# Performance work log

Measured on AMD Instinct MI355X. Metric: run time of the kernel, lower is better.

Reference implementation:

```python
import jax, jax.numpy as jnp
import numpy as np

B, S_IN, S_OUT, D_IN, D_OUT = 8, 1024, 1024, 256, 256
LN_EPS = 1e-5
TWO_PI = 2.0 * np.pi


def setup_inputs() -> dict:
    key = jax.random.key(0)
    ks = jax.random.split(key, 6)
    x = jax.random.normal(ks[0], (B, S_IN, D_IN), dtype=jnp.float32)
    M = jax.random.uniform(ks[1], (D_OUT, D_IN), minval=-0.5, maxval=0.5, dtype=jnp.float32)
    P = jax.random.uniform(ks[2], (D_OUT, D_OUT), minval=-0.1, maxval=0.1, dtype=jnp.float32)
    Linker = jax.random.uniform(ks[3], (S_IN, S_OUT), minval=-0.1, maxval=0.1, dtype=jnp.float32)
    ln_gamma = 1.0 + 0.1 * jax.random.normal(ks[4], (D_OUT,), dtype=jnp.float32)
    ln_beta = 0.1 * jax.random.normal(ks[5], (D_OUT,), dtype=jnp.float32)
    # periods[i, j] = i * out_dim + j + 2  (fixed buffer, non-trainable)
    i = jnp.arange(D_OUT, dtype=jnp.float32)[:, None]
    j = jnp.arange(D_OUT, dtype=jnp.float32)[None, :]
    periods = i * D_OUT + j + 2.0
    return {"x": x, "M": M, "P": P, "Linker": Linker,
            "ln_gamma": ln_gamma, "ln_beta": ln_beta, "periods": periods}


def _layer_norm(z, gamma, beta):
    mu = jnp.mean(z, axis=-1, keepdims=True)
    var = jnp.mean(jnp.square(z - mu), axis=-1, keepdims=True)
    return (z - mu) * jax.lax.rsqrt(var + LN_EPS) * gamma + beta


def reference(x, M, P, Linker, ln_gamma, ln_beta, periods):
    # Projection + LayerNorm: Z [B, S, D]
    Zl = jnp.matmul(x, M.T)
    Z = _layer_norm(Zl, ln_gamma, ln_beta)

    # Position-dependent cos-phase gated reduction:
    # T[b,k,i] = sum_j Z[b,k,j] * P[i,j] * cos(2*pi*k / periods[i,j])
    k = jnp.arange(Z.shape[1], dtype=jnp.float32)  # [S]
    phi = jnp.cos(TWO_PI * k[:, None, None] / periods[None, :, :])  # [S, D, D]
    T = jnp.einsum('bkj,ij,kij->bki', Z, P, phi)

    # Sequence transform via Linker: U[b,s,d] = sum_k T[b,k,d] * Linker[k,s]
    U = jnp.einsum('bkd,ks->bsd', T, Linker)

    # Shared residual: (x @ M^T) through the same Linker
    residual = jnp.einsum('bkd,ks->bsd', Zl, Linker)
    return U + residual
```

## Files before the change

### kernel.cpp

```cpp
#include <hip/hip_runtime.h>
#include <math.h>

#define NB   8
#define SEQ  1024
#define DIM  256

static constexpr float LN_EPS_C = 1e-5f;

typedef __bf16 bfx8 __attribute__((ext_vector_type(8)));
typedef __bf16 bfx4 __attribute__((ext_vector_type(4)));
typedef float  f32v4 __attribute__((ext_vector_type(4)));

__device__ inline void gll16(const void* g, void* l) {
    __builtin_amdgcn_global_load_lds(
        (const __attribute__((address_space(1))) void*)g,
        (__attribute__((address_space(3))) void*)l, 16, 0, 0);
}

__global__ void __launch_bounds__(256)
k_pg1(const float* __restrict__ X, const float* __restrict__ Mw,
      const float* __restrict__ L, const float* __restrict__ P,
      __bf16* __restrict__ Zl, __bf16* __restrict__ Lt, __bf16* __restrict__ Pb)
{
    __shared__ __align__(16) char smraw[65536];
    const int bx = blockIdx.x;
    const int t  = threadIdx.x;

    if (bx >= 768) {
        const int idx = ((bx - 768) * 256 + t) * 4;
        const float4 v = *reinterpret_cast<const float4*>(P + idx);
        bfx4 o;
        o[0] = (__bf16)v.x; o[1] = (__bf16)v.y; o[2] = (__bf16)v.z; o[3] = (__bf16)v.w;
        *reinterpret_cast<bfx4*>(Pb + idx) = o;
        return;
    }
    if (bx >= 512) {
        auto ts = reinterpret_cast<__bf16(*)[72]>(smraw);
        const int b2 = bx - 512;
        const int r0 = (b2 & 15) * 64;
        const int c0 = (b2 >> 4) * 64;
        const int r = t >> 2, cb = (t & 3) * 16;
        const float* sp = L + (size_t)(r0 + r) * SEQ + c0 + cb;
        #pragma unroll
        for (int u = 0; u < 4; ++u) {
            const float4 v = *reinterpret_cast<const float4*>(sp + u * 4);
            ts[r][cb + u*4 + 0] = (__bf16)v.x;
            ts[r][cb + u*4 + 1] = (__bf16)v.y;
            ts[r][cb + u*4 + 2] = (__bf16)v.z;
            ts[r][cb + u*4 + 3] = (__bf16)v.w;
        }
        __syncthreads();
        const int dl = t >> 2, kb = (t & 3) * 16;
        bfx8 o0, o1;
        #pragma unroll
        for (int e = 0; e < 8; ++e) { o0[e] = ts[kb + e][dl]; o1[e] = ts[kb + 8 + e][dl]; }
        __bf16* dp = Lt + (size_t)(c0 + dl) * SEQ + r0 + kb;
        *reinterpret_cast<bfx8*>(dp)     = o0;
        *reinterpret_cast<bfx8*>(dp + 8) = o1;
        return;
    }

    float* AsP = reinterpret_cast<float*>(smraw);
    float* BsP = reinterpret_cast<float*>(smraw + 32768);
    const int m0 = (bx & 127) * 64;
    const int n0 = (bx >> 7) * 64;
    const int l = t & 63, w = t >> 6;
    const int wm = w >> 1, wn = w & 1;

    f32v4 acc[2][2] = {};

    auto stage = [&](int buf, int k0) {
        #pragma unroll
        for (int q = 0; q < 4; ++q) {
            const int p   = 4 * w + q;
            const int row = p * 4 + (l >> 4);
            const int cs  = (l & 15) ^ (row & 15);
            gll16(X  + (size_t)(m0 + row) * 256 + k0 + cs * 4, &AsP[buf*4096 + p*256]);
            gll16(Mw + (size_t)(n0 + row) * 256 + k0 + cs * 4, &BsP[buf*4096 + p*256]);
        }
    };

    stage(0, 0);
    int cur = 0;
    #pragma unroll
    for (int ts_ = 0; ts_ < 4; ++ts_) {
        __syncthreads();
        if (ts_ < 3) stage(cur ^ 1, (ts_ + 1) * 64);
        #pragma unroll
        for (int ks = 0; ks < 2; ++ks) {
            const int c0 = ks * 8 + (l >> 4) * 2;
            const int r15 = l & 15;
            bfx8 af[2], bfr[2];
            #pragma unroll
            for (int i = 0; i < 2; ++i) {
                const int Ra = 32 * wm + 16 * i + (l & 15);
                const float4 f0 = *reinterpret_cast<const float4*>(&AsP[cur*4096 + Ra*64 + (( c0      ^ r15) << 2)]);
                const float4 f1 = *reinterpret_cast<const float4*>(&AsP[cur*4096 + Ra*64 + (((c0 + 1) ^ r15) << 2)]);
                af[i][0]=(__bf16)f0.x; af[i][1]=(__bf16)f0.y; af[i][2]=(__bf16)f0.z; af[i][3]=(__bf16)f0.w;
                af[i][4]=(__bf16)f1.x; af[i][5]=(__bf16)f1.y; af[i][6]=(__bf16)f1.z; af[i][7]=(__bf16)f1.w;
                const int Rb = 32 * wn + 16 * i + (l & 15);
                const float4 g0 = *reinterpret_cast<const float4*>(&BsP[cur*4096 + Rb*64 + (( c0      ^ r15) << 2)]);
                const float4 g1 = *reinterpret_cast<const float4*>(&BsP[cur*4096 + Rb*64 + (((c0 + 1) ^ r15) << 2)]);
                bfr[i][0]=(__bf16)g0.x; bfr[i][1]=(__bf16)g0.y; bfr[i][2]=(__bf16)g0.z; bfr[i][3]=(__bf16)g0.w;
                bfr[i][4]=(__bf16)g1.x; bfr[i][5]=(__bf16)g1.y; bfr[i][6]=(__bf16)g1.z; bfr[i][7]=(__bf16)g1.w;
            }
            #pragma unroll
            for (int i = 0; i < 2; ++i)
                #pragma unroll
                for (int j = 0; j < 2; ++j)
                    acc[i][j] = __builtin_amdgcn_mfma_f32_16x16x32_bf16(af[i], bfr[j], acc[i][j], 0, 0, 0);
        }
        cur ^= 1;
    }

    const int col = l & 15;
    #pragma unroll
    for (int i = 0; i < 2; ++i)
        #pragma unroll
        for (int j = 0; j < 2; ++j)
            #pragma unroll
            for (int r = 0; r < 4; ++r)
                Zl[(size_t)(m0 + 32*wm + 16*i + 4*(l >> 4) + r) * 256 + n0 + 32*wn + 16*j + col]
                    = (__bf16)acc[i][j][r];
}

__global__ void __launch_bounds__(256, 4)
k_gateM(const __bf16* __restrict__ Zl, const __bf16* __restrict__ Pb,
        const float* __restrict__ gamma, const float* __restrict__ beta,
        __bf16* __restrict__ Vt)
{
    __shared__ __bf16 zraw[8 * 256];
    __shared__ __bf16 znorm[16 * 256];
    __shared__ float mu_s[8], rs_s[8];

    const int k = blockIdx.x;
    const int t = threadIdx.x;
    const int l = t & 63, w = t >> 6;

    const int m  = t >> 5;
    const int ch = t & 31;
    const bfx8 zv = *reinterpret_cast<const bfx8*>(Zl + ((size_t)(m * SEQ + k)) * DIM + ch * 8);
    *reinterpret_cast<bfx8*>(&zraw[m * 256 + ((ch ^ m) << 3)]) = zv;

    bfx8 zz;
    #pragma unroll
    for (int e = 0; e < 8; ++e) zz[e] = (__bf16)0.f;
    *reinterpret_cast<bfx8*>(&znorm[(8 + m) * 256 + ((ch ^ m) << 3)]) = zz;

    float s1 = 0.f, s2 = 0.f;
    #pragma unroll
    for (int e = 0; e < 8; ++e) { const float v = (float)zv[e]; s1 += v; s2 += v * v; }
    #pragma unroll
    for (int q = 16; q >= 1; q >>= 1) { s1 += __shfl_xor(s1, q); s2 += __shfl_xor(s2, q); }
    if (ch == 0) {
        const float mu  = s1 * (1.f / DIM);
        const float var = s2 * (1.f / DIM) - mu * mu;
        mu_s[m] = mu;
        rs_s[m] = rsqrtf(var + LN_EPS_C);
    }
    __syncthreads();

    {
        const float mu = mu_s[m], rs = rs_s[m];
        const float4 g0 = *reinterpret_cast<const float4*>(gamma + ch * 8);
        const float4 g1 = *reinterpret_cast<const float4*>(gamma + ch * 8 + 4);
        const float4 b0 = *reinterpret_cast<const float4*>(beta  + ch * 8);
        const float4 b1 = *reinterpret_cast<const float4*>(beta  + ch * 8 + 4);
        const float gv[8] = {g0.x, g0.y, g0.z, g0.w, g1.x, g1.y, g1.z, g1.w};
        const float bv[8] = {b0.x, b0.y, b0.z, b0.w, b1.x, b1.y, b1.z, b1.w};
        bfx8 nv;
        #pragma unroll
        for (int e = 0; e < 8; ++e)
            nv[e] = (__bf16)(((float)zv[e] - mu) * rs * gv[e] + bv[e]);
        *reinterpret_cast<bfx8*>(&znorm[m * 256 + ((ch ^ m) << 3)]) = nv;
    }
    __syncthreads();

    const int mm = l & 15;
    bfx8 af[8];
    #pragma unroll
    for (int ks = 0; ks < 8; ++ks) {
        const int cc = ks * 4 + (l >> 4);
        af[ks] = *reinterpret_cast<const bfx8*>(&znorm[mm * 256 + ((cc ^ (mm & 7)) << 3)]);
    }

    const float kf = (float)k;
    const int n0w = w * 64;
    f32v4 acc[4] = {};
    #pragma unroll
    for (int c = 0; c < 4; ++c) {
        const int i = n0w + 16 * c + (l & 15);
        const __bf16* Prow = Pb + (size_t)i * DIM;
        #pragma unroll
        for (int ks = 0; ks < 8; ++ks) {
            const int jb = ks * 32 + (l >> 4) * 8;
            const bfx8 pv = *reinterpret_cast<const bfx8*>(Prow + jb);
            const float pbase = (float)(i * DIM + jb + 2);
            bfx8 wf;
            #pragma unroll
            for (int e = 0; e < 8; ++e) {
                float r = kf * __builtin_amdgcn_rcpf(pbase + (float)e);
                r = __builtin_amdgcn_fractf(r);
                wf[e] = (__bf16)(__builtin_amdgcn_cosf(r) * (float)pv[e]);
            }
            acc[c] = __builtin_amdgcn_mfma_f32_16x16x32_bf16(af[ks], wf, acc[c], 0, 0, 0);
        }
    }

    const int g = l >> 4;
    if (g < 2) {
        const int col = l & 15;
        #pragma unroll
        for (int c = 0; c < 4; ++c) {
            const int i = n0w + 16 * c + col;
            #pragma unroll
            for (int r = 0; r < 4; ++r) {
                const int b = 4 * g + r;
                const float resid = (float)zraw[b * 256 + (((i >> 3) ^ b) << 3) + (i & 7)];
                Vt[((size_t)(b * DIM + i)) * SEQ + k] = (__bf16)(acc[c][r] + resid);
            }
        }
    }
}

__global__ void __launch_bounds__(256)
k_gemm2(const __bf16* __restrict__ A, const __bf16* __restrict__ Bt,
        float* __restrict__ C)
{
    __shared__ __bf16 As[2][64 * 128];
    __shared__ __bf16 Bs[2][64 * 128];
    const int m0 = blockIdx.x * 64;
    const int n0 = blockIdx.y * 64;
    const long zb = blockIdx.z;
    const int t = threadIdx.x, l = t & 63, w = t >> 6;
    const int wm = w >> 1, wn = w & 1;
    const __bf16* Bz = Bt + zb * (SEQ * DIM);

    f32v4 acc[2][2] = {};

    auto stage = [&](int buf, int k0) {
        #pragma unroll
        for (int q = 0; q < 4; ++q) {
            const int p   = 4 * w + q;
            const int row = p * 4 + (l >> 4);
            const int sc  = (l & 15) ^ (row & 15);
            gll16(A  + (size_t)(m0 + row) * SEQ + k0 + sc * 8, &As[buf][p * 512]);
            gll16(Bz + (size_t)(n0 + row) * SEQ + k0 + sc * 8, &Bs[buf][p * 512]);
        }
    };

    stage(0, 0);
    int cur = 0;
    #pragma unroll
    for (int ts_ = 0; ts_ < 8; ++ts_) {
        __syncthreads();
        if (ts_ < 7) stage(cur ^ 1, (ts_ + 1) * 128);
        #pragma unroll
        for (int ks = 0; ks < 4; ++ks) {
            const int lch = ks * 4 + (l >> 4);
            bfx8 af[2], bfr[2];
            #pragma unroll
            for (int i = 0; i < 2; ++i) {
                const int Ra = 32 * wm + 16 * i + (l & 15);
                af[i]  = *reinterpret_cast<const bfx8*>(&As[cur][Ra * 128 + ((lch ^ (Ra & 15)) << 3)]);
                const int Rb = 32 * wn + 16 * i + (l & 15);
                bfr[i] = *reinterpret_cast<const bfx8*>(&Bs[cur][Rb * 128 + ((lch ^ (Rb & 15)) << 3)]);
            }
            #pragma unroll
            for (int i = 0; i < 2; ++i)
                #pragma unroll
                for (int j = 0; j < 2; ++j)
                    acc[i][j] = __builtin_amdgcn_mfma_f32_16x16x32_bf16(af[i], bfr[j], acc[i][j], 0, 0, 0);
        }
        cur ^= 1;
    }

    const int col = l & 15;
    #pragma unroll
    for (int i = 0; i < 2; ++i)
        #pragma unroll
        for (int j = 0; j < 2; ++j)
            #pragma unroll
            for (int r = 0; r < 4; ++r)
                C[zb * (size_t)(SEQ * DIM)
                  + (size_t)(m0 + 32*wm + 16*i + 4*(l >> 4) + r) * 256
                  + n0 + 32*wn + 16*j + col] = acc[i][j][r];
}

extern "C" void kernel_launch(void* const* d_in, const int* in_sizes, int n_in,
                              void* d_out, int out_size, void* d_ws, size_t ws_size,
                              hipStream_t stream)
{
    const float* x     = (const float*)d_in[0];
    const float* M     = (const float*)d_in[1];
    const float* P     = (const float*)d_in[2];
    const float* L     = (const float*)d_in[3];
    const float* gamma = (const float*)d_in[4];
    const float* beta  = (const float*)d_in[5];
    float* out = (float*)d_out;

    char* ws = (char*)d_ws;
    __bf16* Pb = (__bf16*)(ws);
    __bf16* Lt = (__bf16*)(ws + (128u << 10));
    __bf16* Zl = (__bf16*)(ws + (2u << 20) + (128u << 10));
    __bf16* Vt = (__bf16*)(ws + (6u << 20) + (128u << 10));

    hipLaunchKernelGGL(k_pg1, dim3(832), dim3(256), 0, stream,
                       x, M, L, P, Zl, Lt, Pb);

    hipLaunchKernelGGL(k_gateM, dim3(SEQ), dim3(256), 0, stream,
                       Zl, Pb, gamma, beta, Vt);

    hipLaunchKernelGGL(k_gemm2, dim3(16, 4, 8), dim3(256), 0, stream, Lt, Vt, out);
}
```

Measured before the change: 57.30 us.

## Store gated V row-major and transpose in gemm2 staging; add MFMA priority hints

k_gateM now writes V in [b][k][d] layout, so each block's stores go to contiguous rows instead of a strided transposed layout with SEQ stride. k_gemm2 instead loads V rows into registers and transposes them into swizzled LDS during the loop, overlapping the global load with compute. s_setprio hints are also added around the MFMA blocks in two kernels. The cost is register-staged B loads replacing async global_load_lds, plus extra LDS write work in gemm2.

New measurement: 56.80 us. No clear change (-0.9%).

```diff
diff --git a/kernel.cpp b/kernel.cpp
--- a/kernel.cpp
+++ b/kernel.cpp
@@ -104,11 +104,13 @@
                 bfr[i][0]=(__bf16)g0.x; bfr[i][1]=(__bf16)g0.y; bfr[i][2]=(__bf16)g0.z; bfr[i][3]=(__bf16)g0.w;
                 bfr[i][4]=(__bf16)g1.x; bfr[i][5]=(__bf16)g1.y; bfr[i][6]=(__bf16)g1.z; bfr[i][7]=(__bf16)g1.w;
             }
+            __builtin_amdgcn_s_setprio(1);
             #pragma unroll
             for (int i = 0; i < 2; ++i)
                 #pragma unroll
                 for (int j = 0; j < 2; ++j)
                     acc[i][j] = __builtin_amdgcn_mfma_f32_16x16x32_bf16(af[i], bfr[j], acc[i][j], 0, 0, 0);
+            __builtin_amdgcn_s_setprio(0);
         }
         cur ^= 1;
     }
@@ -127,7 +129,7 @@
 __global__ void __launch_bounds__(256, 4)
 k_gateM(const __bf16* __restrict__ Zl, const __bf16* __restrict__ Pb,
         const float* __restrict__ gamma, const float* __restrict__ beta,
-        __bf16* __restrict__ Vt)
+        __bf16* __restrict__ V)
 {
     __shared__ __bf16 zraw[8 * 256];
     __shared__ __bf16 znorm[16 * 256];
@@ -217,14 +219,14 @@
             for (int r = 0; r < 4; ++r) {
                 const int b = 4 * g + r;
                 const float resid = (float)zraw[b * 256 + (((i >> 3) ^ b) << 3) + (i & 7)];
-                Vt[((size_t)(b * DIM + i)) * SEQ + k] = (__bf16)(acc[c][r] + resid);
+                V[((size_t)(b * SEQ + k)) * DIM + i] = (__bf16)(acc[c][r] + resid);
             }
         }
     }
 }
 
 __global__ void __launch_bounds__(256)
-k_gemm2(const __bf16* __restrict__ A, const __bf16* __restrict__ Bt,
+k_gemm2(const __bf16* __restrict__ A, const __bf16* __restrict__ V,
         float* __restrict__ C)
 {
     __shared__ __bf16 As[2][64 * 128];
@@ -234,27 +236,51 @@
     const long zb = blockIdx.z;
     const int t = threadIdx.x, l = t & 63, w = t >> 6;
     const int wm = w >> 1, wn = w & 1;
-    const __bf16* Bz = Bt + zb * (SEQ * DIM);
+    const __bf16* Vz = V + zb * (SEQ * DIM);
 
     f32v4 acc[2][2] = {};
 
-    auto stage = [&](int buf, int k0) {
+    const int ch = t & 7;
+    const int kq = t >> 3;
+
+    auto stageA = [&](int buf, int k0) {
         #pragma unroll
         for (int q = 0; q < 4; ++q) {
             const int p   = 4 * w + q;
             const int row = p * 4 + (l >> 4);
             const int sc  = (l & 15) ^ (row & 15);
-            gll16(A  + (size_t)(m0 + row) * SEQ + k0 + sc * 8, &As[buf][p * 512]);
-            gll16(Bz + (size_t)(n0 + row) * SEQ + k0 + sc * 8, &Bs[buf][p * 512]);
+            gll16(A + (size_t)(m0 + row) * SEQ + k0 + sc * 8, &As[buf][p * 512]);
         }
     };
 
-    stage(0, 0);
+    bfx8 vbr[4];
+    auto loadB = [&](int k0) {
+        #pragma unroll
+        for (int u = 0; u < 4; ++u)
+            vbr[u] = *reinterpret_cast<const bfx8*>(
+                Vz + (size_t)(k0 + 4 * kq + u) * DIM + n0 + 8 * ch);
+    };
+    auto writeB = [&](int buf) {
+        char* base = (char*)&Bs[buf][0];
+        #pragma unroll
+        for (int e = 0; e < 8; ++e) {
+            const int d = 8 * ch + e;
+            bfx4 o;
+            o[0] = vbr[0][e]; o[1] = vbr[1][e]; o[2] = vbr[2][e]; o[3] = vbr[3][e];
+            *reinterpret_cast<bfx4*>(base + d * 256
+                + (((kq >> 1) ^ (d & 15)) << 4) + (kq & 1) * 8) = o;
+        }
+    };
+
+    stageA(0, 0);
+    loadB(0);
+    writeB(0);
+
     int cur = 0;
     #pragma unroll
     for (int ts_ = 0; ts_ < 8; ++ts_) {
         __syncthreads();
-        if (ts_ < 7) stage(cur ^ 1, (ts_ + 1) * 128);
+        if (ts_ < 7) { stageA(cur ^ 1, (ts_ + 1) * 128); loadB((ts_ + 1) * 128); }
         #pragma unroll
         for (int ks = 0; ks < 4; ++ks) {
             const int lch = ks * 4 + (l >> 4);
@@ -266,12 +292,15 @@
                 const int Rb = 32 * wn + 16 * i + (l & 15);
                 bfr[i] = *reinterpret_cast<const bfx8*>(&Bs[cur][Rb * 128 + ((lch ^ (Rb & 15)) << 3)]);
             }
+            __builtin_amdgcn_s_setprio(1);
             #pragma unroll
             for (int i = 0; i < 2; ++i)
                 #pragma unroll
                 for (int j = 0; j < 2; ++j)
                     acc[i][j] = __builtin_amdgcn_mfma_f32_16x16x32_bf16(af[i], bfr[j], acc[i][j], 0, 0, 0);
-        }
+            __builtin_amdgcn_s_setprio(0);
+        }
+        if (ts_ < 7) writeB(cur ^ 1);
         cur ^= 1;
     }
 
@@ -303,13 +332,14 @@
     __bf16* Pb = (__bf16*)(ws);
     __bf16* Lt = (__bf16*)(ws + (128u << 10));
     __bf16* Zl = (__bf16*)(ws + (2u << 20) + (128u << 10));
-    __bf16* Vt = (__bf16*)(ws + (6u << 20) + (128u << 10));
+    __bf16* V  = (__bf16*)(ws + (6u << 20) + (128u << 10));
 
     hipLaunchKernelGGL(k_pg1, dim3(832), dim3(256), 0, stream,
                        x, M, L, P, Zl, Lt, Pb);
 
     hipLaunchKernelGGL(k_gateM, dim3(SEQ), dim3(256), 0, stream,
-                       Zl, Pb, gamma, beta, Vt);
-
-    hipLaunchKernelGGL(k_gemm2, dim3(16, 4, 8), dim3(256), 0, stream, Lt, Vt, out);
-}
+                       Zl, Pb, gamma, beta, V);
+
+    hipLaunchKernelGGL(k_gemm2, dim3(16, 4, 8), dim3(256), 0, stream,
+                       Lt, V, out);
+}
```
